# Optimization experiments

Hardware: AMD Instinct MI355X
Metric: run time of the kernel (lower is better)

The kernel has to match this reference:

```python
import jax, jax.numpy as jnp
import numpy as np
from jax import lax

B, T, D, H = 256, 1024, 64, 100


def setup_inputs() -> dict:
    key = jax.random.key(0)
    ks = jax.random.split(key, 8)
    s = 1.0 / np.sqrt(H)  # PyTorch LSTM/Linear init scale
    x = jax.random.normal(ks[0], (B, T, D), dtype=jnp.float32)
    h0 = jnp.zeros((1, B, H), dtype=jnp.float32)
    c0 = jnp.zeros((1, B, H), dtype=jnp.float32)
    # PyTorch gate order: i, f, g, o stacked along first dim (4H)
    W_ih = jax.random.uniform(ks[1], (4 * H, D), jnp.float32, -s, s)
    W_hh = jax.random.uniform(ks[2], (4 * H, H), jnp.float32, -s, s)
    b_ih = jax.random.uniform(ks[3], (4 * H,), jnp.float32, -s, s)
    b_hh = jax.random.uniform(ks[4], (4 * H,), jnp.float32, -s, s)
    W_fc = jax.random.uniform(ks[5], (1, H), jnp.float32, -s, s)
    b_fc = jax.random.uniform(ks[6], (1,), jnp.float32, -s, s)
    return {"x": x, "h0": h0, "c0": c0, "W_ih": W_ih, "W_hh": W_hh,
            "b_ih": b_ih, "b_hh": b_hh, "W_fc": W_fc, "b_fc": b_fc}


def reference(x, h0, c0, W_ih, W_hh, b_ih, b_hh, W_fc, b_fc):
    # Precompute input contribution to all gates in one big GEMM: [B,T,4H]
    xg = jnp.einsum('btd,gd->btg', x, W_ih) + (b_ih + b_hh)

    def step(carry, xt):  # xt: [B,4H]
        h, c = carry
        gates = xt + h @ W_hh.T
        i, f, g, o = jnp.split(gates, 4, axis=-1)
        i = jax.nn.sigmoid(i)
        f = jax.nn.sigmoid(f)
        g = jnp.tanh(g)
        o = jax.nn.sigmoid(o)
        c = f * c + i * g
        h = o * jnp.tanh(c)
        return (h, c), None

    (h_T, _), _ = lax.scan(step, (h0[0], c0[0]), jnp.swapaxes(xg, 0, 1))
    # dropout is identity in eval mode; fc head on final hidden state
    out = h_T @ W_fc.T + b_fc  # [B, 1]
    return out
```

## Files before the change

kernel.cpp:

```cpp
#include <hip/hip_runtime.h>
#include <math.h>

#define BATCH 256
#define TSTEPS 1024
#define DIN 64
#define HID 100
#define BLOCK 832
#define XT 32


__global__ __launch_bounds__(BLOCK, 1)
void lstm_fused_kernel(const float* __restrict__ x, const float* __restrict__ h0,
                       const float* __restrict__ c0, const float* __restrict__ W_ih,
                       const float* __restrict__ W_hh, const float* __restrict__ b_ih,
                       const float* __restrict__ b_hh, const float* __restrict__ W_fc,
                       const float* __restrict__ b_fc, float* __restrict__ out)
{
    __shared__ __align__(16) float h_buf[2][104];
    __shared__ __align__(16) float x_tile[XT * DIN];
    __shared__ float red[128];

    const int tid = threadIdx.x;
    const int b = blockIdx.x;
    const int p  = tid & 1;
    const int gq = tid >> 1;
    const int q  = gq & 3;
    const int n  = gq >> 2;
    const int nl = (n < HID) ? n : (HID - 1);
    const int gl = q * HID + nl;

    const int cb  = p * 48;
    const int cb2 = p * 32;

    float whh[52];
    #pragma unroll
    for (int j = 0; j < 52; ++j) whh[j] = W_hh[gl * HID + cb + j];
    if (p) { whh[0] = 0.f; whh[1] = 0.f; whh[2] = 0.f; whh[3] = 0.f; }
    float wih[32];
    #pragma unroll
    for (int j = 0; j < 32; ++j) wih[j] = W_ih[gl * DIN + cb2 + j];
    #pragma unroll
    for (int j = 0; j < 52; ++j) asm volatile("" : "+v"(whh[j]));
    #pragma unroll
    for (int j = 0; j < 32; ++j) asm volatile("" : "+v"(wih[j]));

    const float bias = (p == 0) ? (b_ih[gl] + b_hh[gl]) : 0.f;

    const float mQ = (q == 2) ?  2.f : -1.f;
    const float aQ = (q == 2) ?  1.f :  0.f;
    const float bQ = (q == 2) ? -2.f :  1.f;

    if (tid < HID) h_buf[0][tid] = h0[b * HID + tid];
    float c = 0.f;
    if ((tid & 7) == 0) c = c0[b * HID + nl];
    __syncthreads();

    for (int tt = 0; tt < TSTEPS; tt += XT) {
        if (tid < 512) {
            const float4* xs = reinterpret_cast<const float4*>(
                x + (size_t)b * TSTEPS * DIN + (size_t)tt * DIN);
            reinterpret_cast<float4*>(x_tile)[tid] = xs[tid];
        }
        __syncthreads();

        #pragma unroll 2
        for (int t2 = 0; t2 < XT; ++t2) {
            const int cur = (tt + t2) & 1, nxt = cur ^ 1;

            float a0 = 0.f, a1 = 0.f, a2 = 0.f, a3 = 0.f;
            const float4* h4 = reinterpret_cast<const float4*>(&h_buf[cur][cb]);
            #pragma unroll
            for (int k = 0; k < 13; ++k) {
                float4 hv = h4[k];
                a0 += hv.x * whh[4*k+0];
                a1 += hv.y * whh[4*k+1];
                a2 += hv.z * whh[4*k+2];
                a3 += hv.w * whh[4*k+3];
            }
            const float4* x4 = reinterpret_cast<const float4*>(&x_tile[t2 * DIN + cb2]);
            #pragma unroll
            for (int k = 0; k < 8; ++k) {
                float4 xv = x4[k];
                a0 += xv.x * wih[4*k+0];
                a1 += xv.y * wih[4*k+1];
                a2 += xv.z * wih[4*k+2];
                a3 += xv.w * wih[4*k+3];
            }
            float sum = ((a0 + a1) + (a2 + a3)) + bias;
            float z = sum + __shfl_xor(sum, 1);

            float e = __expf(mQ * z);
            float s = __builtin_amdgcn_rcpf(1.f + e);
            float a = fmaf(bQ, s, aQ);

            float fv = __shfl_down(a, 2);
            float gv = __shfl_down(a, 4);
            float ov = __shfl_down(a, 6);
            if ((tid & 7) == 0) {
                c = fmaf(fv, c, a * gv);
                float e2 = __expf(c + c);
                float th = fmaf(-2.f, __builtin_amdgcn_rcpf(1.f + e2), 1.f);
                h_buf[nxt][n] = ov * th;
            }
            __syncthreads();
        }
    }

    if (tid < HID) red[tid] = h_buf[0][tid] * W_fc[tid];
    __syncthreads();
    if (tid == 0) {
        float sfc = 0.f;
        #pragma unroll 4
        for (int i = 0; i < HID; ++i) sfc += red[i];
        out[b] = sfc + b_fc[0];
    }
}

extern "C" void kernel_launch(void* const* d_in, const int* in_sizes, int n_in,
                              void* d_out, int out_size, void* d_ws, size_t ws_size,
                              hipStream_t stream) {
    const float* x    = (const float*)d_in[0];
    const float* h0   = (const float*)d_in[1];
    const float* c0   = (const float*)d_in[2];
    const float* W_ih = (const float*)d_in[3];
    const float* W_hh = (const float*)d_in[4];
    const float* b_ih = (const float*)d_in[5];
    const float* b_hh = (const float*)d_in[6];
    const float* W_fc = (const float*)d_in[7];
    const float* b_fc = (const float*)d_in[8];
    float* out = (float*)d_out;

    lstm_fused_kernel<<<dim3(BATCH), dim3(BLOCK), 0, stream>>>(
        x, h0, c0, W_ih, W_hh, b_ih, b_hh, W_fc, b_fc, out);
}
```

Before: 927.2 us.

## Use packed fp16 dot2 for LSTM gate matvecs with half-precision hidden state

Converts recurrent and input weights, the hidden state and the x tiles to packed fp16 pairs and computes gate dot products with v_dot2 fp32-accumulate instructions. This halves the FMA count and the LDS reads per timestep and roughly halves weight register use. The final hidden state is kept in a register for the FC head. It adds fp16 rounding of h, x and the weights across 1024 recurrent steps, which risks accuracy drift.

```diff
diff --git a/kernel.cpp b/kernel.cpp
--- a/kernel.cpp
+++ b/kernel.cpp
@@ -7,42 +7,62 @@
 #define HID 100
 #define BLOCK 832
 #define XT 32
+#define HBUF_U32 56
 
+typedef _Float16 f16;
+typedef f16 f16x2 __attribute__((ext_vector_type(2)));
+typedef unsigned int u32;
+
+union UH { u32 u; f16x2 h; };
+
+static __device__ __forceinline__ float dot2u(u32 a, u32 b, float c) {
+    UH ua, ub; ua.u = a; ub.u = b;
+#if __has_builtin(__builtin_amdgcn_fdot2)
+    return __builtin_amdgcn_fdot2(ua.h, ub.h, c, false);
+#else
+    return c + (float)ua.h[0] * (float)ub.h[0] + (float)ua.h[1] * (float)ub.h[1];
+#endif
+}
+static __device__ __forceinline__ u32 pkf(float a, float b) {
+    UH r; r.h[0] = (f16)a; r.h[1] = (f16)b; return r.u;
+}
+static __device__ __forceinline__ float rcpf_(float x) { return __builtin_amdgcn_rcpf(x); }
 
 __global__ __launch_bounds__(BLOCK, 1)
-void lstm_fused_kernel(const float* __restrict__ x, const float* __restrict__ h0,
-                       const float* __restrict__ c0, const float* __restrict__ W_ih,
-                       const float* __restrict__ W_hh, const float* __restrict__ b_ih,
-                       const float* __restrict__ b_hh, const float* __restrict__ W_fc,
-                       const float* __restrict__ b_fc, float* __restrict__ out)
+void lstm_dot2_kernel(const float* __restrict__ x, const float* __restrict__ h0,
+                      const float* __restrict__ c0, const float* __restrict__ W_ih,
+                      const float* __restrict__ W_hh, const float* __restrict__ b_ih,
+                      const float* __restrict__ b_hh, const float* __restrict__ W_fc,
+                      const float* __restrict__ b_fc, float* __restrict__ out)
 {
-    __shared__ __align__(16) float h_buf[2][104];
-    __shared__ __align__(16) float x_tile[XT * DIN];
-    __shared__ float red[128];
+    __shared__ u32 h_lds[2][HBUF_U32];
+    __shared__ u32 x_lds[XT * DIN / 2];
+    __shared__ float red[HID];
 
     const int tid = threadIdx.x;
-    const int b = blockIdx.x;
-    const int p  = tid & 1;
-    const int gq = tid >> 1;
-    const int q  = gq & 3;
-    const int n  = gq >> 2;
-    const int nl = (n < HID) ? n : (HID - 1);
-    const int gl = q * HID + nl;
+    const int b   = blockIdx.x;
+    const int p   = tid & 1;
+    const int gq  = tid >> 1;
+    const int q   = gq & 3;
+    const int n   = gq >> 2;
+    const int nl  = (n < HID) ? n : (HID - 1);
+    const int gl  = q * HID + nl;
+    const int cb  = p * 48;
 
-    const int cb  = p * 48;
-    const int cb2 = p * 32;
-
-    float whh[52];
+    u32 whh[28];
     #pragma unroll
-    for (int j = 0; j < 52; ++j) whh[j] = W_hh[gl * HID + cb + j];
-    if (p) { whh[0] = 0.f; whh[1] = 0.f; whh[2] = 0.f; whh[3] = 0.f; }
-    float wih[32];
+    for (int m = 0; m < 28; ++m) {
+        const int k0 = cb + 2 * m, k1 = k0 + 1;
+        const bool v0 = p ? (k0 >= 52 && k0 < HID) : (k0 < 52);
+        const bool v1 = p ? (k1 >= 52 && k1 < HID) : (k1 < 52);
+        whh[m] = pkf(v0 ? W_hh[gl * HID + k0] : 0.f, v1 ? W_hh[gl * HID + k1] : 0.f);
+    }
+    u32 wih[16];
     #pragma unroll
-    for (int j = 0; j < 32; ++j) wih[j] = W_ih[gl * DIN + cb2 + j];
-    #pragma unroll
-    for (int j = 0; j < 52; ++j) asm volatile("" : "+v"(whh[j]));
-    #pragma unroll
-    for (int j = 0; j < 32; ++j) asm volatile("" : "+v"(wih[j]));
+    for (int m = 0; m < 16; ++m) {
+        const int k0 = p * 32 + 2 * m;
+        wih[m] = pkf(W_ih[gl * DIN + k0], W_ih[gl * DIN + k0 + 1]);
+    }
 
     const float bias = (p == 0) ? (b_ih[gl] + b_hh[gl]) : 0.f;
 
@@ -50,47 +70,55 @@
     const float aQ = (q == 2) ?  1.f :  0.f;
     const float bQ = (q == 2) ? -2.f :  1.f;
 
-    if (tid < HID) h_buf[0][tid] = h0[b * HID + tid];
+    if (tid < HBUF_U32) {
+        const int k = 2 * tid;
+        float v0 = (k     < HID) ? h0[b * HID + k]     : 0.f;
+        float v1 = (k + 1 < HID) ? h0[b * HID + k + 1] : 0.f;
+        h_lds[0][tid] = pkf(v0, v1);
+        h_lds[1][tid] = 0;
+    }
     float c = 0.f;
     if ((tid & 7) == 0) c = c0[b * HID + nl];
+    float hlast = 0.f;
     __syncthreads();
 
     for (int tt = 0; tt < TSTEPS; tt += XT) {
         if (tid < 512) {
-            const float4* xs = reinterpret_cast<const float4*>(
-                x + (size_t)b * TSTEPS * DIN + (size_t)tt * DIN);
-            reinterpret_cast<float4*>(x_tile)[tid] = xs[tid];
+            float4 v = reinterpret_cast<const float4*>(
+                x + (size_t)b * TSTEPS * DIN + (size_t)tt * DIN)[tid];
+            x_lds[2 * tid]     = pkf(v.x, v.y);
+            x_lds[2 * tid + 1] = pkf(v.z, v.w);
         }
         __syncthreads();
 
         #pragma unroll 2
         for (int t2 = 0; t2 < XT; ++t2) {
-            const int cur = (tt + t2) & 1, nxt = cur ^ 1;
+            const int cur = (tt + t2) & 1;
 
             float a0 = 0.f, a1 = 0.f, a2 = 0.f, a3 = 0.f;
-            const float4* h4 = reinterpret_cast<const float4*>(&h_buf[cur][cb]);
+            const uint4* hp = reinterpret_cast<const uint4*>(&h_lds[cur][p * 24]);
             #pragma unroll
-            for (int k = 0; k < 13; ++k) {
-                float4 hv = h4[k];
-                a0 += hv.x * whh[4*k+0];
-                a1 += hv.y * whh[4*k+1];
-                a2 += hv.z * whh[4*k+2];
-                a3 += hv.w * whh[4*k+3];
+            for (int r = 0; r < 7; ++r) {
+                uint4 hv = hp[r];
+                a0 = dot2u(whh[4*r+0], hv.x, a0);
+                a1 = dot2u(whh[4*r+1], hv.y, a1);
+                a2 = dot2u(whh[4*r+2], hv.z, a2);
+                a3 = dot2u(whh[4*r+3], hv.w, a3);
             }
-            const float4* x4 = reinterpret_cast<const float4*>(&x_tile[t2 * DIN + cb2]);
+            const uint4* xp = reinterpret_cast<const uint4*>(&x_lds[t2 * 32 + p * 16]);
             #pragma unroll
-            for (int k = 0; k < 8; ++k) {
-                float4 xv = x4[k];
-                a0 += xv.x * wih[4*k+0];
-                a1 += xv.y * wih[4*k+1];
-                a2 += xv.z * wih[4*k+2];
-                a3 += xv.w * wih[4*k+3];
+            for (int r = 0; r < 4; ++r) {
+                uint4 xv = xp[r];
+                a0 = dot2u(wih[4*r+0], xv.x, a0);
+                a1 = dot2u(wih[4*r+1], xv.y, a1);
+                a2 = dot2u(wih[4*r+2], xv.z, a2);
+                a3 = dot2u(wih[4*r+3], xv.w, a3);
             }
             float sum = ((a0 + a1) + (a2 + a3)) + bias;
             float z = sum + __shfl_xor(sum, 1);
 
             float e = __expf(mQ * z);
-            float s = __builtin_amdgcn_rcpf(1.f + e);
+            float s = rcpf_(1.f + e);
             float a = fmaf(bQ, s, aQ);
 
             float fv = __shfl_down(a, 2);
@@ -99,20 +127,22 @@
             if ((tid & 7) == 0) {
                 c = fmaf(fv, c, a * gv);
                 float e2 = __expf(c + c);
-                float th = fmaf(-2.f, __builtin_amdgcn_rcpf(1.f + e2), 1.f);
-                h_buf[nxt][n] = ov * th;
+                float th = fmaf(-2.f, rcpf_(1.f + e2), 1.f);
+                hlast = ov * th;
+                if (n < HID)
+                    reinterpret_cast<f16*>(&h_lds[cur ^ 1][0])[n] = (f16)hlast;
             }
             __syncthreads();
         }
     }
 
-    if (tid < HID) red[tid] = h_buf[0][tid] * W_fc[tid];
+    if ((tid & 7) == 0 && n < HID) red[n] = hlast * W_fc[n];
     __syncthreads();
     if (tid == 0) {
-        float sfc = 0.f;
+        float s = b_fc[0];
         #pragma unroll 4
-        for (int i = 0; i < HID; ++i) sfc += red[i];
-        out[b] = sfc + b_fc[0];
+        for (int i = 0; i < HID; ++i) s += red[i];
+        out[b] = s;
     }
 }
 
@@ -130,6 +160,6 @@
     const float* b_fc = (const float*)d_in[8];
     float* out = (float*)d_out;
 
-    lstm_fused_kernel<<<dim3(BATCH), dim3(BLOCK), 0, stream>>>(
+    lstm_dot2_kernel<<<dim3(BATCH), dim3(BLOCK), 0, stream>>>(
         x, h0, c0, W_ih, W_hh, b_ih, b_hh, W_fc, b_fc, out);
 }
```

After: 899.4 us. 1.03x faster.
